# Kernel optimization log

Hardware: AMD Instinct MI355X
Metric: run time of the kernel (lower is better)

Reference implementation:

```python
import jax, jax.numpy as jnp
import numpy as np

HID = 256
OUT_DIM = 3


def _nearest_idx(c, size):
    # PyTorch grid_sample nearest, align_corners=False: idx = round(((c+1)*size-1)/2) = floor((c+1)*size/2)
    return jnp.clip(jnp.floor((c + 1.0) * size * 0.5), 0, size - 1).astype(jnp.int32)


def _mlp(x, params):
    # 4 hidden ReLU layers of 256 + linear out (LIIF imnet)
    for w, b in params[:-1]:
        x = jax.nn.relu(x @ w + b)
    w, b = params[-1]
    return x @ w + b


def setup_inputs() -> dict:
    key = jax.random.key(0)
    ks = jax.random.split(key, 16)
    B, C, H, W = 2, 64, 128, 128
    Q = 65536  # 256x256 HR queries
    feat = jax.random.normal(ks[0], (B, C, H, W), dtype=jnp.float32)
    coord = jax.random.uniform(ks[1], (B, Q, 2), dtype=jnp.float32) * 2.0 - 1.0  # in [-1,1)
    cell = jnp.full((B, Q, 2), 2.0 / 256.0, dtype=jnp.float32)
    in_dim = C * 9 + 2 + 2
    dims = [in_dim, HID, HID, HID, HID, OUT_DIM]
    inp = {"feat": feat, "coord": coord, "cell": cell}
    for i in range(5):
        fan_in = dims[i]
        inp[f"w{i}"] = jax.random.normal(ks[2 + 2 * i], (dims[i], dims[i + 1]), dtype=jnp.float32) / np.sqrt(fan_in)
        inp[f"b{i}"] = jnp.zeros((dims[i + 1],), dtype=jnp.float32)
    return inp


def reference(feat, coord, cell, w0, b0, w1, b1, w2, b2, w3, b3, w4, b4):
    params = [(w0, b0), (w1, b1), (w2, b2), (w3, b3), (w4, b4)]
    B, C, H, W = feat.shape
    dt = feat.dtype
    # feat_unfold: F.unfold(feat, 3, padding=1) -> channel order c*9 + (ki*3+kj)
    p = jnp.pad(feat, ((0, 0), (0, 0), (1, 1), (1, 1)))
    feat_u = jnp.stack([p[:, :, i:i + H, j:j + W] for i in range(3) for j in range(3)], axis=2)
    feat_flat = feat_u.reshape(B, C * 9, H * W)  # [B, 576, H*W]

    rx = 1.0 / H  # 2/H/2
    ry = 1.0 / W
    eps_shift = 1e-6
    lim = 1.0 - 1e-6
    rel_cell = cell * jnp.array([H, W], dtype=dt)

    preds, areas = [], []
    for vx in (-1.0, 1.0):
        for vy in (-1.0, 1.0):
            cx = jnp.clip(coord[..., 0] + vx * rx + eps_shift, -lim, lim)
            cy = jnp.clip(coord[..., 1] + vy * ry + eps_shift, -lim, lim)
            ix = _nearest_idx(cx, H)  # coord dim 0 -> height, grid is coord.flip(-1)
            iy = _nearest_idx(cy, W)
            lin = ix * W + iy  # [B, Q]
            q_feat = jnp.take_along_axis(feat_flat, lin[:, None, :], axis=2).transpose(0, 2, 1)  # [B,Q,576]
            # feat_coord grid-center values at the gathered cell (nearest gather of make_coord)
            qx = -1.0 + (2.0 * ix.astype(dt) + 1.0) / H
            qy = -1.0 + (2.0 * iy.astype(dt) + 1.0) / W
            rel = jnp.stack([(coord[..., 0] - qx) * H, (coord[..., 1] - qy) * W], axis=-1)  # [B,Q,2]
            mlp_in = jnp.concatenate([q_feat, rel, rel_cell], axis=-1)  # [B,Q,580]
            preds.append(_mlp(mlp_in, params))  # [B,Q,3]
            areas.append(jnp.abs(rel[..., 0] * rel[..., 1]) + 1e-9)

    # local_ensemble: swap diagonal areas
    areas[0], areas[3] = areas[3], areas[0]
    areas[1], areas[2] = areas[2], areas[1]
    tot = areas[0] + areas[1] + areas[2] + areas[3]
    ret = sum(pr * (a / tot)[..., None] for pr, a in zip(preds, areas))
    return ret
```

## Files before the change

### kernel.cpp

```cpp
#include <hip/hip_runtime.h>

typedef _Float16 half_t;
typedef _Float16 half4 __attribute__((ext_vector_type(4)));
typedef _Float16 half8 __attribute__((ext_vector_type(8)));
typedef float float4v __attribute__((ext_vector_type(4)));

#define MFMA16(a, b, c) __builtin_amdgcn_mfma_f32_16x16x32_f16(a, b, c, 0, 0, 0)

__global__ void pack_all(const float* __restrict__ w0, const float* __restrict__ w1,
                         const float* __restrict__ w2, const float* __restrict__ w3,
                         const float* __restrict__ w4, half_t* __restrict__ w0p,
                         half_t* __restrict__ w1p, half_t* __restrict__ w2p,
                         half_t* __restrict__ w3p, half_t* __restrict__ w4p,
                         half_t* __restrict__ wtp) {
  const int bb = blockIdx.x;
  const float* w;
  half_t* out;
  int K, Nw, nks, base;
  if (bb < 576) {
    w = w0; out = w0p; K = 576; Nw = 256; nks = 18; base = 0;
  } else if (bb < 832) {
    w = w1; out = w1p; K = 256; Nw = 256; nks = 8; base = 576;
  } else if (bb < 1088) {
    w = w2; out = w2p; K = 256; Nw = 256; nks = 8; base = 832;
  } else if (bb < 1344) {
    w = w3; out = w3p; K = 256; Nw = 256; nks = 8; base = 1088;
  } else if (bb < 1360) {
    w = w4; out = w4p; K = 256; Nw = 3; nks = 8; base = 1344;
  } else {
    const int id = threadIdx.x;
#pragma unroll
    for (int e = 0; e < 4; e++) wtp[e * 256 + id] = (half_t)w0[576 * 256 + e * 256 + id];
    return;
  }
  const int id = (bb - base) * 256 + threadIdx.x;
  const int j = id & 7;
  const int lane = (id >> 3) & 63;
  const int t3 = id >> 9;
  const int ks = t3 % nks;
  const int nt = t3 / nks;
  const int n = nt * 16 + (lane & 15);
  const int k = ks * 32 + ((lane >> 4) << 3) + j;
  float v = (k < K && n < Nw) ? w[k * Nw + n] : 0.0f;
  out[id] = (half_t)v;
}

__global__ __launch_bounds__(256, 2) void conv_l0(
    const float* __restrict__ feat, const half_t* __restrict__ w0p,
    const float* __restrict__ b0, half_t* __restrict__ Z) {
  __shared__ alignas(16) half_t Xc[2][64][40];
  const int tid = threadIdx.x;
  const int lane = tid & 63, wave = tid >> 6, quad = lane >> 4, l15 = lane & 15;
  const int blk = blockIdx.x;
  const int b = blk >> 8;
  const int h = (blk >> 1) & 127;
  const int wbase = (blk & 1) << 6;
  const float* featB = feat + b * (64 * 128 * 128);

  auto stage = [&](int ks, int buf) {
#pragma unroll
    for (int e = 0; e < 2; e++) {
      const int idx = e * 256 + tid;
      const int row = idx & 63;
      const int cp = idx >> 6;
      half4 hv;
#pragma unroll
      for (int u = 0; u < 4; u++) {
        const int kk = ks * 32 + cp * 4 + u;
        const int c = kk / 9;
        const int w9 = kk - c * 9;
        const int di = w9 / 3;
        const int dj = w9 - di * 3;
        const int y = h + di - 1;
        const int x = wbase + row + dj - 1;
        float v = 0.0f;
        if ((unsigned)y < 128u && (unsigned)x < 128u) v = featB[(c << 14) + (y << 7) + x];
        hv[u] = (half_t)v;
      }
      *(half4*)(&Xc[buf][row][cp * 4]) = hv;
    }
  };

  const float4v zero4 = {0.0f, 0.0f, 0.0f, 0.0f};
  float4v acc[4][4];
#pragma unroll
  for (int mt = 0; mt < 4; mt++)
#pragma unroll
    for (int jn = 0; jn < 4; jn++) acc[mt][jn] = zero4;

  half8 bcur[4], bnxt[4];
#pragma unroll
  for (int jn = 0; jn < 4; jn++)
    bcur[jn] = *(const half8*)(w0p + ((((wave * 4 + jn) * 18 + 0) * 64 + lane) << 3));
  stage(0, 0);
  __syncthreads();

#pragma unroll 1
  for (int ks = 0; ks < 18; ks++) {
    const int buf = ks & 1;
    if (ks + 1 < 18) {
      stage(ks + 1, buf ^ 1);
#pragma unroll
      for (int jn = 0; jn < 4; jn++)
        bnxt[jn] =
            *(const half8*)(w0p + ((((wave * 4 + jn) * 18 + ks + 1) * 64 + lane) << 3));
    }
    half8 a[4];
#pragma unroll
    for (int mt = 0; mt < 4; mt++)
      a[mt] = *(const half8*)(&Xc[buf][mt * 16 + l15][quad * 8]);
#pragma unroll
    for (int mt = 0; mt < 4; mt++)
#pragma unroll
      for (int jn = 0; jn < 4; jn++)
        acc[mt][jn] = MFMA16(bcur[jn], a[mt], acc[mt][jn]);
#pragma unroll
    for (int jn = 0; jn < 4; jn++) bcur[jn] = bnxt[jn];
    __syncthreads();
  }

  const int posbase = b * 16384 + h * 128 + wbase;
#pragma unroll
  for (int jn = 0; jn < 4; jn++) {
    const float4v bb4 = *(const float4v*)(b0 + wave * 64 + jn * 16 + quad * 4);
#pragma unroll
    for (int mt = 0; mt < 4; mt++) {
      half4 hv;
#pragma unroll
      for (int rr = 0; rr < 4; rr++) hv[rr] = (half_t)(acc[mt][jn][rr] + bb4[rr]);
      *(half4*)(&Z[(size_t)(posbase + mt * 16 + l15) * 256 + wave * 64 + jn * 16 +
                   quad * 4]) = hv;
    }
  }
}

__global__ __launch_bounds__(256, 2) void liif_main(
    const float* __restrict__ coord, const float* __restrict__ cell,
    const half_t* __restrict__ Zp, const half_t* __restrict__ wtp,
    const half_t* __restrict__ w1p, const half_t* __restrict__ w2p,
    const half_t* __restrict__ w3p, const half_t* __restrict__ w4p,
    const float* __restrict__ b1, const float* __restrict__ b2,
    const float* __restrict__ b3, const float* __restrict__ b4,
    float* __restrict__ outp) {
  __shared__ alignas(16) half_t Hs[128][264];
  __shared__ float S4[4][128][4];
  __shared__ int pos4[4][64];
  __shared__ half_t relxh[4][64], relyh[4][64];
  __shared__ half_t cellxh[64], cellyh[64];
  __shared__ float area4[4][64];
  __shared__ float oacc[64][4];
  __shared__ float totv[64];

  const int tid = threadIdx.x;
  const int lane = tid & 63;
  const int wave = tid >> 6;
  const int quad = lane >> 4;
  const int l15 = lane & 15;
  const int blk = blockIdx.x;
  const int batch = blk >> 10;

  {
    const int t = tid >> 6, row = tid & 63;
    const int gq = blk * 64 + row;
    const float cx0 = coord[gq * 2 + 0], cy0 = coord[gq * 2 + 1];
    const float vx = (t & 2) ? 1.0f : -1.0f;
    const float vy = (t & 1) ? 1.0f : -1.0f;
    const float r = 1.0f / 128.0f, lim = 1.0f - 1e-6f, eps = 1e-6f;
    float cx = fminf(fmaxf(cx0 + vx * r + eps, -lim), lim);
    float cy = fminf(fmaxf(cy0 + vy * r + eps, -lim), lim);
    int ix = (int)floorf((cx + 1.0f) * 64.0f);
    ix = min(max(ix, 0), 127);
    int iy = (int)floorf((cy + 1.0f) * 64.0f);
    iy = min(max(iy, 0), 127);
    float qx = -1.0f + (2.0f * ix + 1.0f) * (1.0f / 128.0f);
    float qy = -1.0f + (2.0f * iy + 1.0f) * (1.0f / 128.0f);
    float rxv = (cx0 - qx) * 128.0f;
    float ryv = (cy0 - qy) * 128.0f;
    pos4[t][row] = (batch << 14) + (ix << 7) + iy;
    relxh[t][row] = (half_t)rxv;
    relyh[t][row] = (half_t)ryv;
    area4[t][row] = fabsf(rxv * ryv) + 1e-9f;
    if (t == 0) {
      cellxh[row] = (half_t)(cell[gq * 2 + 0] * 128.0f);
      cellyh[row] = (half_t)(cell[gq * 2 + 1] * 128.0f);
      oacc[row][0] = 0.0f;
      oacc[row][1] = 0.0f;
      oacc[row][2] = 0.0f;
      totv[row] = 0.0f;
    }
  }
  __syncthreads();

  const float4v zero4 = {0.0f, 0.0f, 0.0f, 0.0f};
  const half8 zero8 = {0, 0, 0, 0, 0, 0, 0, 0};
  const int c8 = tid & 31;
  const int rbase = (tid >> 5) * 16;

  const half8 wt0 = *(const half8*)(wtp + 0 * 256 + c8 * 8);
  const half8 wt1 = *(const half8*)(wtp + 1 * 256 + c8 * 8);
  const half8 wt2 = *(const half8*)(wtp + 2 * 256 + c8 * 8);
  const half8 wt3 = *(const half8*)(wtp + 3 * 256 + c8 * 8);

  half8 bcur[4], bnxt[4], bf4[2];
#pragma unroll
  for (int jn = 0; jn < 4; jn++)
    bcur[jn] = *(const half8*)(w1p + ((((wave * 4 + jn) * 8 + 0) * 64 + lane) << 3));

#pragma unroll 1
  for (int p = 0; p < 2; p++) {
#pragma unroll
    for (int e = 0; e < 16; e++) {
      const int r = rbase + e;
      const int corner = 2 * p + (r >> 6);
      const int qrow = r & 63;
      const half8 z = *(const half8*)(Zp + ((size_t)pos4[corner][qrow] << 8) + c8 * 8);
      const half_t rx = relxh[corner][qrow], ry = relyh[corner][qrow];
      const half_t cx = cellxh[qrow], cy = cellyh[qrow];
      const half8 rx8 = {rx, rx, rx, rx, rx, rx, rx, rx};
      const half8 ry8 = {ry, ry, ry, ry, ry, ry, ry, ry};
      const half8 cx8 = {cx, cx, cx, cx, cx, cx, cx, cx};
      const half8 cy8 = {cy, cy, cy, cy, cy, cy, cy, cy};
      half8 v = z + rx8 * wt0 + ry8 * wt1 + cx8 * wt2 + cy8 * wt3;
      v = __builtin_elementwise_max(v, zero8);
      *(half8*)(&Hs[r][c8 * 8]) = v;
    }
    __syncthreads();

    float4v acc[8][4];
#pragma unroll 1
    for (int L = 0; L < 3; L++) {
      const half_t* wp = (L == 0) ? w1p : (L == 1) ? w2p : w3p;
      const float* bp = (L == 0) ? b1 : (L == 1) ? b2 : b3;
#pragma unroll
      for (int mt = 0; mt < 8; mt++)
#pragma unroll
        for (int jn = 0; jn < 4; jn++) acc[mt][jn] = zero4;
#pragma unroll 1
      for (int ks = 0; ks < 8; ks++) {
        if (ks + 1 < 8) {
#pragma unroll
          for (int jn = 0; jn < 4; jn++)
            bnxt[jn] =
                *(const half8*)(wp + ((((wave * 4 + jn) * 8 + ks + 1) * 64 + lane) << 3));
        }
        half8 a[8];
#pragma unroll
        for (int mt = 0; mt < 8; mt++)
          a[mt] = *(const half8*)(&Hs[mt * 16 + l15][ks * 32 + quad * 8]);
#pragma unroll
        for (int mt = 0; mt < 8; mt++)
#pragma unroll
          for (int jn = 0; jn < 4; jn++)
            acc[mt][jn] = MFMA16(bcur[jn], a[mt], acc[mt][jn]);
#pragma unroll
        for (int jn = 0; jn < 4; jn++) bcur[jn] = bnxt[jn];
      }
      __syncthreads();
      if (L < 2) {
        const half_t* wpn = (L == 0) ? w2p : w3p;
#pragma unroll
        for (int jn = 0; jn < 4; jn++)
          bcur[jn] = *(const half8*)(wpn + ((((wave * 4 + jn) * 8 + 0) * 64 + lane) << 3));
      } else {
#pragma unroll
        for (int kx = 0; kx < 2; kx++)
          bf4[kx] = *(const half8*)(w4p + (((wave * 2 + kx) * 64 + lane) << 3));
      }
#pragma unroll
      for (int jn = 0; jn < 4; jn++) {
        const float4v bb4 = *(const float4v*)(bp + wave * 64 + jn * 16 + quad * 4);
#pragma unroll
        for (int mt = 0; mt < 8; mt++) {
          half4 hv;
#pragma unroll
          for (int rr = 0; rr < 4; rr++)
            hv[rr] = (half_t)fmaxf(acc[mt][jn][rr] + bb4[rr], 0.0f);
          *(half4*)(&Hs[mt * 16 + l15][wave * 64 + jn * 16 + quad * 4]) = hv;
        }
      }
      __syncthreads();
    }

    float4v acc4[8];
#pragma unroll
    for (int mt = 0; mt < 8; mt++) acc4[mt] = zero4;
#pragma unroll
    for (int kx = 0; kx < 2; kx++) {
      const int ks = wave * 2 + kx;
#pragma unroll
      for (int mt = 0; mt < 8; mt++) {
        half8 a = *(const half8*)(&Hs[mt * 16 + l15][ks * 32 + quad * 8]);
        acc4[mt] = MFMA16(a, bf4[kx], acc4[mt]);
      }
    }
    if (l15 < 4) {
#pragma unroll
      for (int mt = 0; mt < 8; mt++)
#pragma unroll
        for (int rr = 0; rr < 4; rr++)
          S4[wave][mt * 16 + quad * 4 + rr][l15] = acc4[mt][rr];
    }
    __syncthreads();

    if (p == 0) {
#pragma unroll
      for (int jn = 0; jn < 4; jn++)
        bcur[jn] = *(const half8*)(w1p + ((((wave * 4 + jn) * 8 + 0) * 64 + lane) << 3));
    }

    if (tid < 192) {
      const int qrow = tid / 3;
      const int j = tid - qrow * 3;
      const int ca = 2 * p, cb = 2 * p + 1;
      float pa = b4[j] + S4[0][qrow][j] + S4[1][qrow][j] + S4[2][qrow][j] + S4[3][qrow][j];
      float pb = b4[j] + S4[0][qrow + 64][j] + S4[1][qrow + 64][j] +
                 S4[2][qrow + 64][j] + S4[3][qrow + 64][j];
      oacc[qrow][j] += pa * area4[3 - ca][qrow] + pb * area4[3 - cb][qrow];
    } else if (tid < 256) {
      const int qrow = tid - 192;
      totv[qrow] += area4[2 * p][qrow] + area4[2 * p + 1][qrow];
    }
    __syncthreads();
  }

  if (tid < 192) {
    const int qrow = tid / 3;
    const int j = tid - qrow * 3;
    const int gq = blk * 64 + qrow;
    outp[gq * 3 + j] = oacc[qrow][j] / totv[qrow];
  }
}

extern "C" void kernel_launch(void* const* d_in, const int* in_sizes, int n_in,
                              void* d_out, int out_size, void* d_ws, size_t ws_size,
                              hipStream_t stream) {
  const float* feat = (const float*)d_in[0];
  const float* coord = (const float*)d_in[1];
  const float* cell = (const float*)d_in[2];
  const float* w0 = (const float*)d_in[3];
  const float* b0 = (const float*)d_in[4];
  const float* w1 = (const float*)d_in[5];
  const float* b1 = (const float*)d_in[6];
  const float* w2 = (const float*)d_in[7];
  const float* b2 = (const float*)d_in[8];
  const float* w3 = (const float*)d_in[9];
  const float* b3 = (const float*)d_in[10];
  const float* w4 = (const float*)d_in[11];
  const float* b4 = (const float*)d_in[12];

  half_t* w0p = (half_t*)d_ws;
  half_t* w1p = w0p + 147456;
  half_t* w2p = w1p + 65536;
  half_t* w3p = w2p + 65536;
  half_t* w4p = w3p + 65536;
  half_t* wtp = w4p + 4096;
  half_t* Z = (half_t*)d_ws + 524288;

  pack_all<<<1361, 256, 0, stream>>>(w0, w1, w2, w3, w4, w0p, w1p, w2p, w3p, w4p, wtp);
  conv_l0<<<512, 256, 0, stream>>>(feat, w0p, b0, Z);
  liif_main<<<2048, 256, 0, stream>>>(coord, cell, Z, wtp, w1p, w2p, w3p, w4p, b1, b2,
                                      b3, b4, (float*)d_out);
}
```

Before: 336.7 us.

## Permute K ordering of packed weights to vectorize conv staging and epilogue stores

Reorders the reduction dimension of layer-0 weights so each k-step covers one 3x3 offset and 32 channels, which makes the conv input staging contiguous per channel group with one bounds check. It also applies a permutation to the hidden-layer weight rows so the epilogues can write 16 contiguous halves (two half8 stores) instead of four half4 stores. The weight packing kernel now uses shared-memory transposes with far fewer blocks, and the running area-total accumulation is replaced by a final sum. Correctness depends on the sigma permutation matching the new activation layout consistently across all layers.

```diff
diff --git a/kernel.cpp b/kernel.cpp
--- a/kernel.cpp
+++ b/kernel.cpp
@@ -7,42 +7,68 @@
 
 #define MFMA16(a, b, c) __builtin_amdgcn_mfma_f32_16x16x32_f16(a, b, c, 0, 0, 0)
 
-__global__ void pack_all(const float* __restrict__ w0, const float* __restrict__ w1,
-                         const float* __restrict__ w2, const float* __restrict__ w3,
-                         const float* __restrict__ w4, half_t* __restrict__ w0p,
-                         half_t* __restrict__ w1p, half_t* __restrict__ w2p,
-                         half_t* __restrict__ w3p, half_t* __restrict__ w4p,
-                         half_t* __restrict__ wtp) {
+__device__ __host__ __forceinline__ int sigma_p(int s) {
+  return (s & 0xC3) | ((s & 0x0C) << 2) | ((s & 0x30) >> 2);
+}
+
+__global__ __launch_bounds__(256) void pack_frags(
+    const float* __restrict__ w0, const float* __restrict__ w1,
+    const float* __restrict__ w2, const float* __restrict__ w3,
+    const float* __restrict__ w4, half_t* __restrict__ w0p,
+    half_t* __restrict__ w1p, half_t* __restrict__ w2p,
+    half_t* __restrict__ w3p, half_t* __restrict__ w4p,
+    half_t* __restrict__ wtp) {
   const int bb = blockIdx.x;
+  const int tid = threadIdx.x;
+  if (bb == 42) {
+#pragma unroll
+    for (int e = 0; e < 16; e++) {
+      const int id = e * 256 + tid;
+      const int j = id & 7;
+      const int lane = (id >> 3) & 63;
+      const int ks = id >> 9;
+      const int n = lane & 15;
+      const int k = ks * 32 + ((lane >> 4) << 3) + j;
+      w4p[id] = (half_t)((n < 3) ? w4[sigma_p(k) * 3 + n] : 0.0f);
+    }
+#pragma unroll
+    for (int e = 0; e < 4; e++)
+      wtp[e * 256 + tid] = (half_t)w0[576 * 256 + e * 256 + sigma_p(tid)];
+    return;
+  }
+  __shared__ float Wt[32][260];
   const float* w;
   half_t* out;
-  int K, Nw, nks, base;
-  if (bb < 576) {
-    w = w0; out = w0p; K = 576; Nw = 256; nks = 18; base = 0;
-  } else if (bb < 832) {
-    w = w1; out = w1p; K = 256; Nw = 256; nks = 8; base = 576;
-  } else if (bb < 1088) {
-    w = w2; out = w2p; K = 256; Nw = 256; nks = 8; base = 832;
-  } else if (bb < 1344) {
-    w = w3; out = w3p; K = 256; Nw = 256; nks = 8; base = 1088;
-  } else if (bb < 1360) {
-    w = w4; out = w4p; K = 256; Nw = 3; nks = 8; base = 1344;
-  } else {
-    const int id = threadIdx.x;
-#pragma unroll
-    for (int e = 0; e < 4; e++) wtp[e * 256 + id] = (half_t)w0[576 * 256 + e * 256 + id];
-    return;
-  }
-  const int id = (bb - base) * 256 + threadIdx.x;
-  const int j = id & 7;
-  const int lane = (id >> 3) & 63;
-  const int t3 = id >> 9;
-  const int ks = t3 % nks;
-  const int nt = t3 / nks;
-  const int n = nt * 16 + (lane & 15);
-  const int k = ks * 32 + ((lane >> 4) << 3) + j;
-  float v = (k < K && n < Nw) ? w[k * Nw + n] : 0.0f;
-  out[id] = (half_t)v;
+  int nks, ks;
+  int mode;
+  if (bb < 18) { w = w0; out = w0p; nks = 18; ks = bb; mode = 0; }
+  else if (bb < 26) { w = w1; out = w1p; nks = 8; ks = bb - 18; mode = 1; }
+  else if (bb < 34) { w = w2; out = w2p; nks = 8; ks = bb - 26; mode = 1; }
+  else { w = w3; out = w3p; nks = 8; ks = bb - 34; mode = 1; }
+  {
+    const int n4 = (tid & 63) * 4;
+    const int kr = tid >> 6;
+#pragma unroll
+    for (int e = 0; e < 8; e++) {
+      const int kp = e * 4 + kr;
+      int kg = ks * 32 + kp;
+      if (mode == 0) { const int w9 = kg >> 6, c = kg & 63; kg = c * 9 + w9; }
+      else kg = sigma_p(kg);
+      *(float4v*)&Wt[kp][n4] = *(const float4v*)(w + (size_t)kg * 256 + n4);
+    }
+  }
+  __syncthreads();
+  const int lane = tid & 63;
+  const int l15 = lane & 15;
+  const int kq = (lane >> 4) << 3;
+#pragma unroll
+  for (int e = 0; e < 4; e++) {
+    const int nt = e * 4 + (tid >> 6);
+    half8 hv;
+#pragma unroll
+    for (int j = 0; j < 8; j++) hv[j] = (half_t)Wt[kq + j][nt * 16 + l15];
+    *(half8*)&out[((nt * nks + ks) * 64 + lane) * 8] = hv;
+  }
 }
 
 __global__ __launch_bounds__(256, 2) void conv_l0(
@@ -58,27 +84,22 @@
   const float* featB = feat + b * (64 * 128 * 128);
 
   auto stage = [&](int ks, int buf) {
-#pragma unroll
-    for (int e = 0; e < 2; e++) {
-      const int idx = e * 256 + tid;
-      const int row = idx & 63;
-      const int cp = idx >> 6;
-      half4 hv;
-#pragma unroll
-      for (int u = 0; u < 4; u++) {
-        const int kk = ks * 32 + cp * 4 + u;
-        const int c = kk / 9;
-        const int w9 = kk - c * 9;
-        const int di = w9 / 3;
-        const int dj = w9 - di * 3;
-        const int y = h + di - 1;
-        const int x = wbase + row + dj - 1;
-        float v = 0.0f;
-        if ((unsigned)y < 128u && (unsigned)x < 128u) v = featB[(c << 14) + (y << 7) + x];
-        hv[u] = (half_t)v;
-      }
-      *(half4*)(&Xc[buf][row][cp * 4]) = hv;
-    }
+    const int w9 = ks >> 1;
+    const int di = w9 / 3;
+    const int dj = w9 - 3 * di;
+    const int pos = tid & 63;
+    const int grp = tid >> 6;
+    const int y = h + di - 1;
+    const int x = wbase + pos + dj - 1;
+    const bool ok = ((unsigned)y < 128u) && ((unsigned)x < 128u);
+    const float* base = featB + (((ks & 1) * 32 + grp * 8) << 14) + (y << 7) + x;
+    half4 h0, h1;
+#pragma unroll
+    for (int u = 0; u < 4; u++) h0[u] = (half_t)(ok ? base[u << 14] : 0.0f);
+#pragma unroll
+    for (int u = 0; u < 4; u++) h1[u] = (half_t)(ok ? base[(u + 4) << 14] : 0.0f);
+    *(half4*)&Xc[buf][pos][grp * 8] = h0;
+    *(half4*)&Xc[buf][pos][grp * 8 + 4] = h1;
   };
 
   const float4v zero4 = {0.0f, 0.0f, 0.0f, 0.0f};
@@ -119,18 +140,24 @@
     __syncthreads();
   }
 
+  float4v bb[4];
+#pragma unroll
+  for (int jn = 0; jn < 4; jn++)
+    bb[jn] = *(const float4v*)(b0 + (wave * 4 + jn) * 16 + quad * 4);
   const int posbase = b * 16384 + h * 128 + wbase;
 #pragma unroll
-  for (int jn = 0; jn < 4; jn++) {
-    const float4v bb4 = *(const float4v*)(b0 + wave * 64 + jn * 16 + quad * 4);
-#pragma unroll
-    for (int mt = 0; mt < 4; mt++) {
-      half4 hv;
-#pragma unroll
-      for (int rr = 0; rr < 4; rr++) hv[rr] = (half_t)(acc[mt][jn][rr] + bb4[rr]);
-      *(half4*)(&Z[(size_t)(posbase + mt * 16 + l15) * 256 + wave * 64 + jn * 16 +
-                   quad * 4]) = hv;
-    }
+  for (int mt = 0; mt < 4; mt++) {
+    half8 o0, o1;
+#pragma unroll
+    for (int jn = 0; jn < 2; jn++)
+#pragma unroll
+      for (int rr = 0; rr < 4; rr++) {
+        o0[jn * 4 + rr] = (half_t)(acc[mt][jn][rr] + bb[jn][rr]);
+        o1[jn * 4 + rr] = (half_t)(acc[mt][jn + 2][rr] + bb[jn + 2][rr]);
+      }
+    half_t* zp = &Z[(size_t)(posbase + mt * 16 + l15) * 256 + wave * 64 + quad * 16];
+    *(half8*)zp = o0;
+    *(half8*)(zp + 8) = o1;
   }
 }
 
@@ -149,7 +176,6 @@
   __shared__ half_t cellxh[64], cellyh[64];
   __shared__ float area4[4][64];
   __shared__ float oacc[64][4];
-  __shared__ float totv[64];
 
   const int tid = threadIdx.x;
   const int lane = tid & 63;
@@ -186,7 +212,6 @@
       oacc[row][0] = 0.0f;
       oacc[row][1] = 0.0f;
       oacc[row][2] = 0.0f;
-      totv[row] = 0.0f;
     }
   }
   __syncthreads();
@@ -266,17 +291,23 @@
         for (int kx = 0; kx < 2; kx++)
           bf4[kx] = *(const half8*)(w4p + (((wave * 2 + kx) * 64 + lane) << 3));
       }
-#pragma unroll
-      for (int jn = 0; jn < 4; jn++) {
-        const float4v bb4 = *(const float4v*)(bp + wave * 64 + jn * 16 + quad * 4);
-#pragma unroll
-        for (int mt = 0; mt < 8; mt++) {
-          half4 hv;
-#pragma unroll
-          for (int rr = 0; rr < 4; rr++)
-            hv[rr] = (half_t)fmaxf(acc[mt][jn][rr] + bb4[rr], 0.0f);
-          *(half4*)(&Hs[mt * 16 + l15][wave * 64 + jn * 16 + quad * 4]) = hv;
-        }
+      float4v bb[4];
+#pragma unroll
+      for (int jn = 0; jn < 4; jn++)
+        bb[jn] = *(const float4v*)(bp + (wave * 4 + jn) * 16 + quad * 4);
+#pragma unroll
+      for (int mt = 0; mt < 8; mt++) {
+        half8 o0, o1;
+#pragma unroll
+        for (int jn = 0; jn < 2; jn++)
+#pragma unroll
+          for (int rr = 0; rr < 4; rr++) {
+            o0[jn * 4 + rr] = (half_t)fmaxf(acc[mt][jn][rr] + bb[jn][rr], 0.0f);
+            o1[jn * 4 + rr] = (half_t)fmaxf(acc[mt][jn + 2][rr] + bb[jn + 2][rr], 0.0f);
+          }
+        half_t* hp = &Hs[mt * 16 + l15][wave * 64 + quad * 16];
+        *(half8*)hp = o0;
+        *(half8*)(hp + 8) = o1;
       }
       __syncthreads();
     }
@@ -316,9 +347,6 @@
       float pb = b4[j] + S4[0][qrow + 64][j] + S4[1][qrow + 64][j] +
                  S4[2][qrow + 64][j] + S4[3][qrow + 64][j];
       oacc[qrow][j] += pa * area4[3 - ca][qrow] + pb * area4[3 - cb][qrow];
-    } else if (tid < 256) {
-      const int qrow = tid - 192;
-      totv[qrow] += area4[2 * p][qrow] + area4[2 * p + 1][qrow];
     }
     __syncthreads();
   }
@@ -326,8 +354,9 @@
   if (tid < 192) {
     const int qrow = tid / 3;
     const int j = tid - qrow * 3;
-    const int gq = blk * 64 + qrow;
-    outp[gq * 3 + j] = oacc[qrow][j] / totv[qrow];
+    const float tot =
+        area4[0][qrow] + area4[1][qrow] + area4[2][qrow] + area4[3][qrow];
+    outp[(blk * 64 + qrow) * 3 + j] = oacc[qrow][j] / tot;
   }
 }
 
@@ -356,7 +385,7 @@
   half_t* wtp = w4p + 4096;
   half_t* Z = (half_t*)d_ws + 524288;
 
-  pack_all<<<1361, 256, 0, stream>>>(w0, w1, w2, w3, w4, w0p, w1p, w2p, w3p, w4p, wtp);
+  pack_frags<<<43, 256, 0, stream>>>(w0, w1, w2, w3, w4, w0p, w1p, w2p, w3p, w4p, wtp);
   conv_l0<<<512, 256, 0, stream>>>(feat, w0p, b0, Z);
   liif_main<<<2048, 256, 0, stream>>>(coord, cell, Z, wtp, w1p, w2p, w3p, w4p, b1, b2,
                                       b3, b4, (float*)d_out);
```

Result: faster. 326.4 us (-3.1%).
